# Kernel tuning notes

Measured on AMD Instinct MI355X. Metric: run time of the kernel, lower is better.

Reference implementation:

```python
import jax, jax.numpy as jnp
import numpy as np

NEG_SLOPE = 0.01  # torch leaky_relu default

N_NODES = 100000
N_EDGES = 1600000
D = 64
N_BBOX = 4096


def setup_inputs() -> dict:
    key = jax.random.key(0)
    ks = jax.random.split(key, 9)
    x = jax.random.normal(ks[0], (N_NODES, D), dtype=jnp.float32)
    edge_index = jax.random.randint(ks[1], (2, N_EDGES), 0, N_NODES, dtype=jnp.int64)
    bbox = jax.random.randint(ks[2], (N_BBOX,), 0, N_NODES, dtype=jnp.int64)
    s = 1.0 / np.sqrt(D)
    W1_rel = jax.random.normal(ks[3], (D, D), dtype=jnp.float32) * s
    b1 = jax.random.normal(ks[4], (D,), dtype=jnp.float32) * s
    W1_root = jax.random.normal(ks[5], (D, D), dtype=jnp.float32) * s
    W2_rel = jax.random.normal(ks[6], (D, D), dtype=jnp.float32) * s
    b2 = jax.random.normal(ks[7], (D,), dtype=jnp.float32) * s
    W2_root = jax.random.normal(ks[8], (D, D), dtype=jnp.float32) * s
    return {"x": x, "edge_index": edge_index, "bbox": bbox,
            "W1_rel": W1_rel, "b1": b1, "W1_root": W1_root,
            "W2_rel": W2_rel, "b2": b2, "W2_root": W2_root}


def graph_conv(x, src, dst, W_rel, b, W_root):
    # PyG GraphConv: out_i = W_rel @ (sum_{j in N(i)} x_j) + b + W_root @ x_i
    msg = x[src]                                        # [E, D] gather
    agg = jax.ops.segment_sum(msg, dst, num_segments=x.shape[0])  # [N, D] scatter-add
    return agg @ W_rel + b + x @ W_root


def reference(x, edge_index, bbox, W1_rel, b1, W1_root, W2_rel, b2, W2_root):
    src, dst = edge_index[0], edge_index[1]
    h = graph_conv(x, src, dst, W1_rel, b1, W1_root)
    h = jax.nn.leaky_relu(h, NEG_SLOPE)
    # dropout is identity at inference (training=False)
    h = graph_conv(h, src, dst, W2_rel, b2, W2_root)
    h = jax.nn.leaky_relu(h, NEG_SLOPE)
    return h[bbox]
```

## Files before the change

kernel.cpp:

```cpp
#include <hip/hip_runtime.h>

#define N_NODES 100000
#define N_EDGES 1600000
#define D 64
#define N_BBOX 4096
#define CAP 64
#define NBITW 3136
#define SLICE 12500
#define NBLK_A 6250
#define SEGCAP 96

typedef short bf16x8 __attribute__((ext_vector_type(8)));
typedef float f32x4 __attribute__((ext_vector_type(4)));

__device__ __forceinline__ float readlane_f(float v, int l) {
  return __int_as_float(__builtin_amdgcn_readlane(__float_as_int(v), l));
}
__device__ __forceinline__ int bperm(int srclane, int v) {
  return __builtin_amdgcn_ds_bpermute(srclane << 2, v);
}
__device__ __forceinline__ float lrelu(float v) {
  return fmaxf(v, 0.01f * v);
}
__device__ __forceinline__ bool testbit(const unsigned* bits, int i) {
  return (bits[i >> 5] >> (i & 31)) & 1u;
}
__device__ __forceinline__ short f2bf(float f) {
  unsigned u = __float_as_uint(f);
  u += 0x7FFFu + ((u >> 16) & 1u);
  return (short)(u >> 16);
}
__device__ __forceinline__ float bf2f(short s) {
  return __uint_as_float(((unsigned)(unsigned short)s) << 16);
}

__global__ __launch_bounds__(256) void prep_kernel(const float4* __restrict__ x4,
                                                   bf16x8* __restrict__ xb,
                                                   const int* __restrict__ bbox,
                                                   unsigned* __restrict__ is_bbox_bits,
                                                   unsigned* __restrict__ needed_bits,
                                                   int* __restrict__ cnt) {
  const int i = blockIdx.x * 256 + threadIdx.x;
  if (i < N_NODES) cnt[i] = 0;
  if (i < N_NODES * 8) {
    const float4 a = x4[i * 2], b = x4[i * 2 + 1];
    bf16x8 r;
    r[0] = f2bf(a.x); r[1] = f2bf(a.y); r[2] = f2bf(a.z); r[3] = f2bf(a.w);
    r[4] = f2bf(b.x); r[5] = f2bf(b.y); r[6] = f2bf(b.z); r[7] = f2bf(b.w);
    xb[i] = r;
  } else {
    const int t = i - N_NODES * 8;
    if (t < N_BBOX) {
      const int n = bbox[t];
      const unsigned m = 1u << (n & 31);
      atomicOr(&is_bbox_bits[n >> 5], m);
      atomicOr(&needed_bits[n >> 5], m);
    }
  }
}

__global__ __launch_bounds__(256) void scan_kernel(const int* __restrict__ src,
                                                   const int* __restrict__ dst,
                                                   const unsigned* __restrict__ is_bbox_bits,
                                                   unsigned* __restrict__ needed_bits,
                                                   int* __restrict__ qcnt,
                                                   int* __restrict__ qseg) {
  __shared__ int lcnt[8];
  __shared__ int lbuf[8 * SEGCAP];
  const int t = threadIdx.x;
  const int lane = t & 63;
  const int e = blockIdx.x * 256 + t;
  if (t < 8) lcnt[t] = 0;
  __syncthreads();

  const int d = dst[e];
  const int s = src[e];
  if (testbit(is_bbox_bits, d)) {
    atomicOr(&needed_bits[s >> 5], 1u << (s & 31));
  }
  const int q = d / SLICE;
  const int pv = s | ((d - q * SLICE) << 17);
#pragma unroll
  for (int qq = 0; qq < 8; qq++) {
    const unsigned long long mask = __ballot(q == qq);
    if (!mask) continue;
    const int nq = __popcll(mask);
    const int leader = (int)__builtin_ctzll(mask);
    int base = 0;
    if (lane == leader) base = atomicAdd(&lcnt[qq], nq);
    base = __builtin_amdgcn_readlane(base, leader);
    if (q == qq) {
      const int p = base + __popcll(mask & ((1ull << lane) - 1ull));
      if (p < SEGCAP) lbuf[qq * SEGCAP + p] = pv;
    }
  }
  __syncthreads();

  const size_t segbase = (size_t)blockIdx.x * 8;
  if (t < 8) qcnt[segbase + t] = (lcnt[t] > SEGCAP) ? SEGCAP : lcnt[t];
  for (int i = t; i < 8 * SEGCAP; i += 256) {
    const int q2 = i / SEGCAP, p2 = i - q2 * SEGCAP;
    if (p2 < lcnt[q2]) qseg[(segbase + q2) * SEGCAP + p2] = lbuf[i];
  }
}

__global__ __launch_bounds__(256) void scatterB_kernel(const int* __restrict__ qcnt,
                                                       const int* __restrict__ qseg,
                                                       const unsigned* __restrict__ needed_bits,
                                                       int* __restrict__ cnt,
                                                       int* __restrict__ slots) {
  const int sl = blockIdx.x & 7;
  const int bidx = blockIdx.x >> 3;
  const int nblk = gridDim.x >> 3;
  const int base_node = sl * SLICE;
  const int sub = threadIdx.x >> 4;
  const int pp = threadIdx.x & 15;

  for (int b0 = bidx * 16; b0 < NBLK_A; b0 += nblk * 16) {
    const int b = b0 + sub;
    if (b >= NBLK_A) continue;
    const int n = qcnt[(size_t)b * 8 + sl];
    const int* seg = qseg + ((size_t)b * 8 + sl) * SEGCAP;
    for (int p = pp; p < n; p += 16) {
      const int pv = seg[p];
      const int d = base_node + (pv >> 17);
      if (!testbit(needed_bits, d)) continue;
      const int pos = atomicAdd(&cnt[d], 1);
      if (pos < CAP) slots[(size_t)d * CAP + pos] = pv & 0x1FFFF;
    }
  }
}

__global__ __launch_bounds__(256) void gather1_kernel(const uint4* __restrict__ xb,
                                                      const unsigned* __restrict__ needed_bits,
                                                      const int* __restrict__ cnt,
                                                      const int* __restrict__ slots,
                                                      bf16x8* __restrict__ aggb) {
  const int wid = (blockIdx.x * blockDim.x + threadIdx.x) >> 6;
  if (wid >= N_NODES) return;
  if (!testbit(needed_bits, wid)) return;
  const int lane = threadIdx.x & 63;
  const int g = lane >> 3, c = lane & 7;

  int n = cnt[wid];
  n = (n > CAP) ? CAP : n;
  const int myslot = (lane < n) ? slots[(size_t)wid * CAP + lane] : 0;

  float accf[8] = {0.f, 0.f, 0.f, 0.f, 0.f, 0.f, 0.f, 0.f};
  for (int e0 = 0; e0 < n; e0 += 64) {
    int idx[8], s[8];
    uint4 v[8];
#pragma unroll
    for (int u = 0; u < 8; u++) {
      idx[u] = e0 + u * 8 + g;
      s[u] = bperm(idx[u], myslot);
    }
#pragma unroll
    for (int u = 0; u < 8; u++) {
      v[u] = make_uint4(0u, 0u, 0u, 0u);
      if (idx[u] < n) v[u] = xb[(size_t)s[u] * 8 + c];
    }
#pragma unroll
    for (int u = 0; u < 8; u++) {
      accf[0] += __uint_as_float(v[u].x << 16);
      accf[1] += __uint_as_float(v[u].x & 0xFFFF0000u);
      accf[2] += __uint_as_float(v[u].y << 16);
      accf[3] += __uint_as_float(v[u].y & 0xFFFF0000u);
      accf[4] += __uint_as_float(v[u].z << 16);
      accf[5] += __uint_as_float(v[u].z & 0xFFFF0000u);
      accf[6] += __uint_as_float(v[u].w << 16);
      accf[7] += __uint_as_float(v[u].w & 0xFFFF0000u);
    }
  }
#pragma unroll
  for (int off = 8; off < 64; off <<= 1)
#pragma unroll
    for (int i = 0; i < 8; i++) accf[i] += __shfl_xor(accf[i], off);

  if (lane < 8) {
    bf16x8 r;
#pragma unroll
    for (int i = 0; i < 8; i++) r[i] = f2bf(accf[i]);
    aggb[(size_t)wid * 8 + lane] = r;
  }
}

__global__ __launch_bounds__(256, 1) void dense1_mfma_kernel(
    const short* __restrict__ xb, const short* __restrict__ aggb,
    const float* __restrict__ W1rel, const float* __restrict__ b1,
    const float* __restrict__ W1root, short* __restrict__ hb) {
  const int lane = threadIdx.x & 63;
  const int cn = lane & 15;
  const int quad = lane >> 4;
  const int wid0 = (blockIdx.x * blockDim.x + threadIdx.x) >> 6;
  const int nwaves = (gridDim.x * blockDim.x) >> 6;

  bf16x8 brel[2][4], broot[2][4];
#pragma unroll
  for (int kh = 0; kh < 2; kh++)
#pragma unroll
    for (int nt = 0; nt < 4; nt++)
#pragma unroll
      for (int i = 0; i < 8; i++) {
        const int k = kh * 32 + quad * 8 + i;
        brel[kh][nt][i] = f2bf(W1rel[k * D + nt * 16 + cn]);
        broot[kh][nt][i] = f2bf(W1root[k * D + nt * 16 + cn]);
      }
  float bj[4];
#pragma unroll
  for (int nt = 0; nt < 4; nt++) bj[nt] = b1[nt * 16 + cn];

  for (int tile = wid0; tile < N_NODES / 16; tile += nwaves) {
    const int node0 = tile * 16;
    const short* arow = aggb + (size_t)(node0 + cn) * D;
    const short* xrow = xb + (size_t)(node0 + cn) * D;

    f32x4 acc[4] = {};
#pragma unroll
    for (int kh = 0; kh < 2; kh++) {
      const int kb = kh * 32 + quad * 8;
      const bf16x8 a_agg = *(const bf16x8*)(arow + kb);
      const bf16x8 a_x = *(const bf16x8*)(xrow + kb);
#pragma unroll
      for (int nt = 0; nt < 4; nt++) {
        acc[nt] = __builtin_amdgcn_mfma_f32_16x16x32_bf16(a_agg, brel[kh][nt],
                                                          acc[nt], 0, 0, 0);
        acc[nt] = __builtin_amdgcn_mfma_f32_16x16x32_bf16(a_x, broot[kh][nt],
                                                          acc[nt], 0, 0, 0);
      }
    }
#pragma unroll
    for (int nt = 0; nt < 4; nt++) {
#pragma unroll
      for (int r = 0; r < 4; r++) {
        const int row = quad * 4 + r;
        hb[(size_t)(node0 + row) * D + nt * 16 + cn] = f2bf(lrelu(acc[nt][r] + bj[nt]));
      }
    }
  }
}

__global__ __launch_bounds__(256, 1) void layer2_kernel(
    const uint4* __restrict__ hb4, const int* __restrict__ cnt,
    const int* __restrict__ slots, const int* __restrict__ bbox,
    const float* __restrict__ W2rel, const float* __restrict__ b2,
    const float* __restrict__ W2root, float* __restrict__ out) {
  const int t = (blockIdx.x * blockDim.x + threadIdx.x) >> 6;
  if (t >= N_BBOX) return;
  const int lane = threadIdx.x & 63;
  const int g = lane >> 3, c = lane & 7;

  float wrel[D], wroot[D];
#pragma unroll
  for (int k = 0; k < D; k++) {
    wrel[k] = W2rel[k * D + lane];
    wroot[k] = W2root[k * D + lane];
  }
  const float bj = b2[lane];

  const int node = __builtin_amdgcn_readfirstlane(bbox[t]);
  int n = cnt[node];
  n = (n > CAP) ? CAP : n;
  const int myslot = (lane < n) ? slots[(size_t)node * CAP + lane] : 0;

  float accf[8] = {0.f, 0.f, 0.f, 0.f, 0.f, 0.f, 0.f, 0.f};
  for (int e0 = 0; e0 < n; e0 += 64) {
    int idx[8], s[8];
    uint4 v[8];
#pragma unroll
    for (int u = 0; u < 8; u++) {
      idx[u] = e0 + u * 8 + g;
      s[u] = bperm(idx[u], myslot);
    }
#pragma unroll
    for (int u = 0; u < 8; u++) {
      v[u] = make_uint4(0u, 0u, 0u, 0u);
      if (idx[u] < n) v[u] = hb4[(size_t)s[u] * 8 + c];
    }
#pragma unroll
    for (int u = 0; u < 8; u++) {
      accf[0] += __uint_as_float(v[u].x << 16);
      accf[1] += __uint_as_float(v[u].x & 0xFFFF0000u);
      accf[2] += __uint_as_float(v[u].y << 16);
      accf[3] += __uint_as_float(v[u].y & 0xFFFF0000u);
      accf[4] += __uint_as_float(v[u].z << 16);
      accf[5] += __uint_as_float(v[u].z & 0xFFFF0000u);
      accf[6] += __uint_as_float(v[u].w << 16);
      accf[7] += __uint_as_float(v[u].w & 0xFFFF0000u);
    }
  }
#pragma unroll
  for (int off = 8; off < 64; off <<= 1)
#pragma unroll
    for (int i = 0; i < 8; i++) accf[i] += __shfl_xor(accf[i], off);

  const float hi = bf2f(((const short*)hb4)[(size_t)node * D + lane]);
  float s0 = 0.f, s1 = 0.f, s2 = 0.f, s3 = 0.f;
#pragma unroll
  for (int k = 0; k < D; k += 2) {
    const float a0 = readlane_f(accf[k & 7], k >> 3);
    const float a1 = readlane_f(accf[(k + 1) & 7], (k + 1) >> 3);
    s0 += a0 * wrel[k];
    s1 += readlane_f(hi, k) * wroot[k];
    s2 += a1 * wrel[k + 1];
    s3 += readlane_f(hi, k + 1) * wroot[k + 1];
  }
  out[(size_t)t * D + lane] = lrelu(bj + ((s0 + s1) + (s2 + s3)));
}


extern "C" void kernel_launch(void* const* d_in, const int* in_sizes, int n_in,
                              void* d_out, int out_size, void* d_ws, size_t ws_size,
                              hipStream_t stream) {
  const float* x = (const float*)d_in[0];
  const int* ei = (const int*)d_in[1];
  const int* src = ei;
  const int* dst = ei + N_EDGES;
  const int* bbox = (const int*)d_in[2];
  const float* W1rel = (const float*)d_in[3];
  const float* b1 = (const float*)d_in[4];
  const float* W1root = (const float*)d_in[5];
  const float* W2rel = (const float*)d_in[6];
  const float* b2 = (const float*)d_in[7];
  const float* W2root = (const float*)d_in[8];
  float* out = (float*)d_out;

  char* ws = (char*)d_ws;
  size_t off = 0;
  auto alloc = [&](size_t bytes) -> char* {
    char* p = ws + off;
    off = (off + bytes + 511) & ~(size_t)511;
    return p;
  };
  unsigned* is_bbox_bits = (unsigned*)alloc(NBITW * sizeof(unsigned));
  unsigned* needed_bits = (unsigned*)alloc(NBITW * sizeof(unsigned));
  char* zero_end = ws + off;
  int* cnt = (int*)alloc(N_NODES * sizeof(int));
  int* qcnt = (int*)alloc((size_t)NBLK_A * 8 * sizeof(int));
  int* qseg = (int*)alloc((size_t)NBLK_A * 8 * SEGCAP * sizeof(int));
  int* slots = (int*)alloc((size_t)N_NODES * CAP * sizeof(int));
  short* xb = (short*)alloc((size_t)N_NODES * D * sizeof(short));
  short* aggb = (short*)alloc((size_t)N_NODES * D * sizeof(short));
  short* hb = (short*)alloc((size_t)N_NODES * D * sizeof(short));

  hipMemsetAsync(is_bbox_bits, 0, (size_t)(zero_end - (char*)is_bbox_bits), stream);
  prep_kernel<<<(N_NODES * 8 + N_BBOX + 255) / 256, 256, 0, stream>>>(
      (const float4*)x, (bf16x8*)xb, bbox, is_bbox_bits, needed_bits, cnt);
  scan_kernel<<<NBLK_A, 256, 0, stream>>>(src, dst, is_bbox_bits, needed_bits,
                                          qcnt, qseg);
  scatterB_kernel<<<2048, 256, 0, stream>>>(qcnt, qseg, needed_bits, cnt, slots);
  gather1_kernel<<<(N_NODES + 3) / 4, 256, 0, stream>>>(
      (const uint4*)xb, needed_bits, cnt, slots, (bf16x8*)aggb);
  dense1_mfma_kernel<<<512, 256, 0, stream>>>(xb, aggb, W1rel, b1, W1root, hb);
  layer2_kernel<<<(N_BBOX + 3) / 4, 256, 0, stream>>>(
      (const uint4*)hb, cnt, slots, bbox, W2rel, b2, W2root, out);
}
```

Measured before the change: 193.4 us.

## Fuse layer-1 gather with MFMA dense and use MFMA for layer-2 bbox rows

The separate layer-1 gather and dense kernels become one kernel. Each block gathers 16 node rows into an LDS tile, then runs a 16x16 MFMA per wave, and only nodes marked as needed get their h rows written. This removes the aggb round trip through global memory and one launch. The layer-2 kernel now processes 16 bbox nodes per block with MFMA instead of per-lane register FMAs with readlane, at the cost of bf16 rounding of the aggregate and per-tile __syncthreads with serial per-row gathers inside each wave.

```diff
diff --git a/kernel.cpp b/kernel.cpp
--- a/kernel.cpp
+++ b/kernel.cpp
@@ -9,13 +9,12 @@
 #define SLICE 12500
 #define NBLK_A 6250
 #define SEGCAP 96
+#define NTILE1 (N_NODES / 16)
+#define NTILE2 (N_BBOX / 16)
 
 typedef short bf16x8 __attribute__((ext_vector_type(8)));
 typedef float f32x4 __attribute__((ext_vector_type(4)));
 
-__device__ __forceinline__ float readlane_f(float v, int l) {
-  return __int_as_float(__builtin_amdgcn_readlane(__float_as_int(v), l));
-}
 __device__ __forceinline__ int bperm(int srclane, int v) {
   return __builtin_amdgcn_ds_bpermute(srclane << 2, v);
 }
@@ -29,9 +28,6 @@
   unsigned u = __float_as_uint(f);
   u += 0x7FFFu + ((u >> 16) & 1u);
   return (short)(u >> 16);
-}
-__device__ __forceinline__ float bf2f(short s) {
-  return __uint_as_float(((unsigned)(unsigned short)s) << 16);
 }
 
 __global__ __launch_bounds__(256) void prep_kernel(const float4* __restrict__ x4,
@@ -131,22 +127,14 @@
   }
 }
 
-__global__ __launch_bounds__(256) void gather1_kernel(const uint4* __restrict__ xb,
-                                                      const unsigned* __restrict__ needed_bits,
-                                                      const int* __restrict__ cnt,
-                                                      const int* __restrict__ slots,
-                                                      bf16x8* __restrict__ aggb) {
-  const int wid = (blockIdx.x * blockDim.x + threadIdx.x) >> 6;
-  if (wid >= N_NODES) return;
-  if (!testbit(needed_bits, wid)) return;
-  const int lane = threadIdx.x & 63;
+__device__ __forceinline__ void gather_rows(const uint4* __restrict__ rows,
+                                            const int* __restrict__ slots,
+                                            int node, int n, int lane,
+                                            float accf[8]) {
   const int g = lane >> 3, c = lane & 7;
-
-  int n = cnt[wid];
-  n = (n > CAP) ? CAP : n;
-  const int myslot = (lane < n) ? slots[(size_t)wid * CAP + lane] : 0;
-
-  float accf[8] = {0.f, 0.f, 0.f, 0.f, 0.f, 0.f, 0.f, 0.f};
+  const int myslot = (lane < n) ? slots[(size_t)node * CAP + lane] : 0;
+#pragma unroll
+  for (int i = 0; i < 8; i++) accf[i] = 0.f;
   for (int e0 = 0; e0 < n; e0 += 64) {
     int idx[8], s[8];
     uint4 v[8];
@@ -158,7 +146,7 @@
 #pragma unroll
     for (int u = 0; u < 8; u++) {
       v[u] = make_uint4(0u, 0u, 0u, 0u);
-      if (idx[u] < n) v[u] = xb[(size_t)s[u] * 8 + c];
+      if (idx[u] < n) v[u] = rows[(size_t)s[u] * 8 + c];
     }
 #pragma unroll
     for (int u = 0; u < 8; u++) {
@@ -176,136 +164,144 @@
   for (int off = 8; off < 64; off <<= 1)
 #pragma unroll
     for (int i = 0; i < 8; i++) accf[i] += __shfl_xor(accf[i], off);
-
-  if (lane < 8) {
-    bf16x8 r;
-#pragma unroll
-    for (int i = 0; i < 8; i++) r[i] = f2bf(accf[i]);
-    aggb[(size_t)wid * 8 + lane] = r;
-  }
-}
-
-__global__ __launch_bounds__(256, 1) void dense1_mfma_kernel(
-    const short* __restrict__ xb, const short* __restrict__ aggb,
-    const float* __restrict__ W1rel, const float* __restrict__ b1,
-    const float* __restrict__ W1root, short* __restrict__ hb) {
-  const int lane = threadIdx.x & 63;
-  const int cn = lane & 15;
-  const int quad = lane >> 4;
-  const int wid0 = (blockIdx.x * blockDim.x + threadIdx.x) >> 6;
-  const int nwaves = (gridDim.x * blockDim.x) >> 6;
-
-  bf16x8 brel[2][4], broot[2][4];
+}
+
+__global__ __launch_bounds__(256) void gd1_kernel(
+    const uint4* __restrict__ xb4, const short* __restrict__ xb,
+    const unsigned* __restrict__ needed_bits, const int* __restrict__ cnt,
+    const int* __restrict__ slots, const float* __restrict__ W1rel,
+    const float* __restrict__ b1, const float* __restrict__ W1root,
+    short* __restrict__ hb) {
+  __shared__ __align__(16) short aggt[16][72];
+  const int t = threadIdx.x;
+  const int lane = t & 63;
+  const int wid = t >> 6;
+  const int cn = lane & 15, quad = lane >> 4;
+
+  bf16x8 brel[2], broot[2];
 #pragma unroll
   for (int kh = 0; kh < 2; kh++)
 #pragma unroll
-    for (int nt = 0; nt < 4; nt++)
-#pragma unroll
-      for (int i = 0; i < 8; i++) {
-        const int k = kh * 32 + quad * 8 + i;
-        brel[kh][nt][i] = f2bf(W1rel[k * D + nt * 16 + cn]);
-        broot[kh][nt][i] = f2bf(W1root[k * D + nt * 16 + cn]);
+    for (int i = 0; i < 8; i++) {
+      const int k = kh * 32 + quad * 8 + i;
+      brel[kh][i] = f2bf(W1rel[k * D + wid * 16 + cn]);
+      broot[kh][i] = f2bf(W1root[k * D + wid * 16 + cn]);
+    }
+  const float bj = b1[wid * 16 + cn];
+
+  for (int tile = blockIdx.x; tile < NTILE1; tile += gridDim.x) {
+    const int node0 = tile * 16;
+#pragma unroll
+    for (int r4 = 0; r4 < 4; r4++) {
+      const int row = wid * 4 + r4;
+      const int node = node0 + row;
+      int n = cnt[node];
+      n = (n > CAP) ? CAP : n;
+      if (n == 0) {
+        if (lane < 8) {
+          bf16x8 z = {0, 0, 0, 0, 0, 0, 0, 0};
+          *(bf16x8*)(&aggt[row][lane * 8]) = z;
+        }
+        continue;
       }
-  float bj[4];
-#pragma unroll
-  for (int nt = 0; nt < 4; nt++) bj[nt] = b1[nt * 16 + cn];
-
-  for (int tile = wid0; tile < N_NODES / 16; tile += nwaves) {
-    const int node0 = tile * 16;
-    const short* arow = aggb + (size_t)(node0 + cn) * D;
-    const short* xrow = xb + (size_t)(node0 + cn) * D;
-
-    f32x4 acc[4] = {};
+      float accf[8];
+      gather_rows(xb4, slots, node, n, lane, accf);
+      if (lane < 8) {
+        bf16x8 r;
+#pragma unroll
+        for (int i = 0; i < 8; i++) r[i] = f2bf(accf[i]);
+        *(bf16x8*)(&aggt[row][lane * 8]) = r;
+      }
+    }
+    __syncthreads();
+    const int mrow = node0 + cn;
+    const bool ndrow = testbit(needed_bits, mrow);
+    f32x4 acc = {};
 #pragma unroll
     for (int kh = 0; kh < 2; kh++) {
-      const int kb = kh * 32 + quad * 8;
-      const bf16x8 a_agg = *(const bf16x8*)(arow + kb);
-      const bf16x8 a_x = *(const bf16x8*)(xrow + kb);
-#pragma unroll
-      for (int nt = 0; nt < 4; nt++) {
-        acc[nt] = __builtin_amdgcn_mfma_f32_16x16x32_bf16(a_agg, brel[kh][nt],
-                                                          acc[nt], 0, 0, 0);
-        acc[nt] = __builtin_amdgcn_mfma_f32_16x16x32_bf16(a_x, broot[kh][nt],
-                                                          acc[nt], 0, 0, 0);
+      const bf16x8 a_agg = *(const bf16x8*)(&aggt[cn][kh * 32 + quad * 8]);
+      bf16x8 a_x = {0, 0, 0, 0, 0, 0, 0, 0};
+      if (ndrow)
+        a_x = *(const bf16x8*)(xb + (size_t)mrow * D + kh * 32 + quad * 8);
+      acc = __builtin_amdgcn_mfma_f32_16x16x32_bf16(a_agg, brel[kh], acc, 0, 0, 0);
+      acc = __builtin_amdgcn_mfma_f32_16x16x32_bf16(a_x, broot[kh], acc, 0, 0, 0);
+    }
+#pragma unroll
+    for (int r = 0; r < 4; r++) {
+      const int row = quad * 4 + r;
+      if (testbit(needed_bits, node0 + row))
+        hb[(size_t)(node0 + row) * D + wid * 16 + cn] = f2bf(lrelu(acc[r] + bj));
+    }
+    __syncthreads();
+  }
+}
+
+__global__ __launch_bounds__(256) void gd2_kernel(
+    const uint4* __restrict__ hb4, const short* __restrict__ hb,
+    const int* __restrict__ cnt, const int* __restrict__ slots,
+    const int* __restrict__ bbox, const float* __restrict__ W2rel,
+    const float* __restrict__ b2, const float* __restrict__ W2root,
+    float* __restrict__ out) {
+  __shared__ __align__(16) short aggt[16][72];
+  __shared__ int nodes_s[16];
+  const int t = threadIdx.x;
+  const int lane = t & 63;
+  const int wid = t >> 6;
+  const int cn = lane & 15, quad = lane >> 4;
+  const int t0 = blockIdx.x * 16;
+
+  if (t < 16) nodes_s[t] = bbox[t0 + t];
+
+  bf16x8 brel[2], broot[2];
+#pragma unroll
+  for (int kh = 0; kh < 2; kh++)
+#pragma unroll
+    for (int i = 0; i < 8; i++) {
+      const int k = kh * 32 + quad * 8 + i;
+      brel[kh][i] = f2bf(W2rel[k * D + wid * 16 + cn]);
+      broot[kh][i] = f2bf(W2root[k * D + wid * 16 + cn]);
+    }
+  const float bj = b2[wid * 16 + cn];
+  __syncthreads();
+
+#pragma unroll
+  for (int r4 = 0; r4 < 4; r4++) {
+    const int row = wid * 4 + r4;
+    const int node = nodes_s[row];
+    int n = cnt[node];
+    n = (n > CAP) ? CAP : n;
+    if (n == 0) {
+      if (lane < 8) {
+        bf16x8 z = {0, 0, 0, 0, 0, 0, 0, 0};
+        *(bf16x8*)(&aggt[row][lane * 8]) = z;
       }
-    }
-#pragma unroll
-    for (int nt = 0; nt < 4; nt++) {
-#pragma unroll
-      for (int r = 0; r < 4; r++) {
-        const int row = quad * 4 + r;
-        hb[(size_t)(node0 + row) * D + nt * 16 + cn] = f2bf(lrelu(acc[nt][r] + bj[nt]));
-      }
-    }
-  }
-}
-
-__global__ __launch_bounds__(256, 1) void layer2_kernel(
-    const uint4* __restrict__ hb4, const int* __restrict__ cnt,
-    const int* __restrict__ slots, const int* __restrict__ bbox,
-    const float* __restrict__ W2rel, const float* __restrict__ b2,
-    const float* __restrict__ W2root, float* __restrict__ out) {
-  const int t = (blockIdx.x * blockDim.x + threadIdx.x) >> 6;
-  if (t >= N_BBOX) return;
-  const int lane = threadIdx.x & 63;
-  const int g = lane >> 3, c = lane & 7;
-
-  float wrel[D], wroot[D];
-#pragma unroll
-  for (int k = 0; k < D; k++) {
-    wrel[k] = W2rel[k * D + lane];
-    wroot[k] = W2root[k * D + lane];
-  }
-  const float bj = b2[lane];
-
-  const int node = __builtin_amdgcn_readfirstlane(bbox[t]);
-  int n = cnt[node];
-  n = (n > CAP) ? CAP : n;
-  const int myslot = (lane < n) ? slots[(size_t)node * CAP + lane] : 0;
-
-  float accf[8] = {0.f, 0.f, 0.f, 0.f, 0.f, 0.f, 0.f, 0.f};
-  for (int e0 = 0; e0 < n; e0 += 64) {
-    int idx[8], s[8];
-    uint4 v[8];
-#pragma unroll
-    for (int u = 0; u < 8; u++) {
-      idx[u] = e0 + u * 8 + g;
-      s[u] = bperm(idx[u], myslot);
-    }
-#pragma unroll
-    for (int u = 0; u < 8; u++) {
-      v[u] = make_uint4(0u, 0u, 0u, 0u);
-      if (idx[u] < n) v[u] = hb4[(size_t)s[u] * 8 + c];
-    }
-#pragma unroll
-    for (int u = 0; u < 8; u++) {
-      accf[0] += __uint_as_float(v[u].x << 16);
-      accf[1] += __uint_as_float(v[u].x & 0xFFFF0000u);
-      accf[2] += __uint_as_float(v[u].y << 16);
-      accf[3] += __uint_as_float(v[u].y & 0xFFFF0000u);
-      accf[4] += __uint_as_float(v[u].z << 16);
-      accf[5] += __uint_as_float(v[u].z & 0xFFFF0000u);
-      accf[6] += __uint_as_float(v[u].w << 16);
-      accf[7] += __uint_as_float(v[u].w & 0xFFFF0000u);
-    }
-  }
-#pragma unroll
-  for (int off = 8; off < 64; off <<= 1)
-#pragma unroll
-    for (int i = 0; i < 8; i++) accf[i] += __shfl_xor(accf[i], off);
-
-  const float hi = bf2f(((const short*)hb4)[(size_t)node * D + lane]);
-  float s0 = 0.f, s1 = 0.f, s2 = 0.f, s3 = 0.f;
-#pragma unroll
-  for (int k = 0; k < D; k += 2) {
-    const float a0 = readlane_f(accf[k & 7], k >> 3);
-    const float a1 = readlane_f(accf[(k + 1) & 7], (k + 1) >> 3);
-    s0 += a0 * wrel[k];
-    s1 += readlane_f(hi, k) * wroot[k];
-    s2 += a1 * wrel[k + 1];
-    s3 += readlane_f(hi, k + 1) * wroot[k + 1];
-  }
-  out[(size_t)t * D + lane] = lrelu(bj + ((s0 + s1) + (s2 + s3)));
+      continue;
+    }
+    float accf[8];
+    gather_rows(hb4, slots, node, n, lane, accf);
+    if (lane < 8) {
+      bf16x8 r;
+#pragma unroll
+      for (int i = 0; i < 8; i++) r[i] = f2bf(accf[i]);
+      *(bf16x8*)(&aggt[row][lane * 8]) = r;
+    }
+  }
+  __syncthreads();
+
+  const int rnode = nodes_s[cn];
+  f32x4 acc = {};
+#pragma unroll
+  for (int kh = 0; kh < 2; kh++) {
+    const bf16x8 a_agg = *(const bf16x8*)(&aggt[cn][kh * 32 + quad * 8]);
+    const bf16x8 a_h = *(const bf16x8*)(hb + (size_t)rnode * D + kh * 32 + quad * 8);
+    acc = __builtin_amdgcn_mfma_f32_16x16x32_bf16(a_agg, brel[kh], acc, 0, 0, 0);
+    acc = __builtin_amdgcn_mfma_f32_16x16x32_bf16(a_h, broot[kh], acc, 0, 0, 0);
+  }
+#pragma unroll
+  for (int r = 0; r < 4; r++) {
+    const int row = quad * 4 + r;
+    out[(size_t)(t0 + row) * D + wid * 16 + cn] = lrelu(acc[r] + bj);
+  }
 }
 
 
@@ -340,7 +336,6 @@
   int* qseg = (int*)alloc((size_t)NBLK_A * 8 * SEGCAP * sizeof(int));
   int* slots = (int*)alloc((size_t)N_NODES * CAP * sizeof(int));
   short* xb = (short*)alloc((size_t)N_NODES * D * sizeof(short));
-  short* aggb = (short*)alloc((size_t)N_NODES * D * sizeof(short));
   short* hb = (short*)alloc((size_t)N_NODES * D * sizeof(short));
 
   hipMemsetAsync(is_bbox_bits, 0, (size_t)(zero_end - (char*)is_bbox_bits), stream);
@@ -349,9 +344,8 @@
   scan_kernel<<<NBLK_A, 256, 0, stream>>>(src, dst, is_bbox_bits, needed_bits,
                                           qcnt, qseg);
   scatterB_kernel<<<2048, 256, 0, stream>>>(qcnt, qseg, needed_bits, cnt, slots);
-  gather1_kernel<<<(N_NODES + 3) / 4, 256, 0, stream>>>(
-      (const uint4*)xb, needed_bits, cnt, slots, (bf16x8*)aggb);
-  dense1_mfma_kernel<<<512, 256, 0, stream>>>(xb, aggb, W1rel, b1, W1root, hb);
-  layer2_kernel<<<(N_BBOX + 3) / 4, 256, 0, stream>>>(
-      (const uint4*)hb, cnt, slots, bbox, W2rel, b2, W2root, out);
-}
+  gd1_kernel<<<2048, 256, 0, stream>>>((const uint4*)xb, xb, needed_bits, cnt,
+                                       slots, W1rel, b1, W1root, hb);
+  gd2_kernel<<<NTILE2, 256, 0, stream>>>((const uint4*)hb, hb, cnt, slots, bbox,
+                                         W2rel, b2, W2root, out);
+}
```

Result: slower. 201.1 us (+4.0%).
